# Kernel optimization log

Hardware: AMD Instinct MI355X
Metric: run time of the kernel (lower is better)

The kernel has to match this reference:

```python
import jax, jax.numpy as jnp
import numpy as np

N_NODES = 100000
N_EDGES = 1600000
IN_DIM = 128
OUT_DIM = 32
N_HEADS = 4


def setup_inputs() -> dict:
    key = jax.random.key(0)
    k1, k2, k3, k4, k5 = jax.random.split(key, 5)
    x = jax.random.normal(k1, (N_NODES, IN_DIM), dtype=jnp.float32)
    edge_index = jax.random.randint(k2, (2, N_EDGES), 0, N_NODES, dtype=jnp.int64)
    # torch nn.Linear weight layout: [out_features, in_features]
    W = jax.random.normal(k3, (OUT_DIM * N_HEADS, IN_DIM), dtype=jnp.float32) * (1.0 / np.sqrt(IN_DIM))
    a_left = jax.random.normal(k4, (N_HEADS, OUT_DIM), dtype=jnp.float32) * 0.01
    a_right = jax.random.normal(k5, (N_HEADS, OUT_DIM), dtype=jnp.float32) * 0.01
    return {"x": x, "edge_index": edge_index, "W": W, "a_left": a_left, "a_right": a_right}


def reference(x, edge_index, W, a_left, a_right):
    N = x.shape[0]
    H, D = a_left.shape
    # h: [N, H, D]
    h = (x @ W.T).reshape(N, H, D)
    src = edge_index[0]
    dst = edge_index[1]
    h_src = h[src]                                   # [E, H, D] gather
    h_dst = h[dst]                                   # [E, H, D] gather
    e = jnp.einsum('ehd,hd->eh', h_src, a_left) + jnp.einsum('ehd,hd->eh', h_dst, a_right)
    e = jax.nn.leaky_relu(e, negative_slope=0.2)
    e_exp = jnp.exp(e)                               # faithful: no max-subtraction, as in source
    denom = jax.ops.segment_sum(e_exp, dst, num_segments=N)   # [N, H]
    alpha = e_exp / (denom[dst] + 1e-8)              # [E, H]
    weighted = h_src * alpha[:, :, None]             # [E, H, D]
    out = jax.ops.segment_sum(weighted, dst, num_segments=N)  # [N, H, D]
    return out.reshape(N, H * D)                     # concat=True
```

## Files before the change

### kernel.cpp

```cpp
#include <hip/hip_runtime.h>
#include <hip/hip_bf16.h>


constexpr int IN_DIM = 128;
constexpr int HD     = 128;
constexpr int CSHIFT = 10;
constexpr int CCAP   = 17408;
constexpr int CPAD   = 16;

typedef float f32x4 __attribute__((ext_vector_type(4)));

__device__ __forceinline__ unsigned short f2bf(float f) {
  __hip_bfloat16 b = __float2bfloat16(f);
  return *(unsigned short*)&b;
}
__device__ __forceinline__ float bfl(unsigned u) { return __uint_as_float(u << 16); }
__device__ __forceinline__ float bfh(unsigned u) { return __uint_as_float(u & 0xffff0000u); }

__global__ __launch_bounds__(256)
void gemm_k(const float* __restrict__ x, const float* __restrict__ W,
            const float* __restrict__ a_left, const float* __restrict__ a_right,
            unsigned int* __restrict__ hb,
            float* __restrict__ el, float* __restrict__ er,
            int N) {
  __shared__ float xs[32][132];
  __shared__ float ws[32][132];
  const int tid = threadIdx.x;
  const int tx = tid & 15, ty = tid >> 4;
  const int n0 = blockIdx.x * 128;

  float acc[8][8];
#pragma unroll
  for (int i = 0; i < 8; ++i)
#pragma unroll
    for (int j = 0; j < 8; ++j) acc[i][j] = 0.f;

  for (int kc = 0; kc < IN_DIM; kc += 32) {
#pragma unroll
    for (int i = 0; i < 4; ++i) {
      int f  = tid + 256 * i;
      int r  = f >> 3;
      int k4 = f & 7;
      float4 xv = make_float4(0.f, 0.f, 0.f, 0.f);
      int node = n0 + r;
      if (node < N) xv = *(const float4*)&x[(size_t)node * IN_DIM + kc + 4 * k4];
      xs[4*k4+0][r] = xv.x; xs[4*k4+1][r] = xv.y; xs[4*k4+2][r] = xv.z; xs[4*k4+3][r] = xv.w;
      float4 wv = *(const float4*)&W[(size_t)r * IN_DIM + kc + 4 * k4];
      ws[4*k4+0][r] = wv.x; ws[4*k4+1][r] = wv.y; ws[4*k4+2][r] = wv.z; ws[4*k4+3][r] = wv.w;
    }
    __syncthreads();
#pragma unroll 8
    for (int kk = 0; kk < 32; ++kk) {
      float4 xa = *(const float4*)&xs[kk][8 * ty];
      float4 xb = *(const float4*)&xs[kk][8 * ty + 4];
      float4 wa = *(const float4*)&ws[kk][4 * tx];
      float4 wb = *(const float4*)&ws[kk][64 + 4 * tx];
      float xr[8] = {xa.x, xa.y, xa.z, xa.w, xb.x, xb.y, xb.z, xb.w};
      float wr[8] = {wa.x, wa.y, wa.z, wa.w, wb.x, wb.y, wb.z, wb.w};
#pragma unroll
      for (int i = 0; i < 8; ++i)
#pragma unroll
        for (int j = 0; j < 8; ++j) acc[i][j] += xr[i] * wr[j];
    }
    __syncthreads();
  }

  const int headA = tx >> 3;
  const int headB = 2 + (tx >> 3);
  const int co    = 4 * (tx & 7);
  float alA[4], arA[4], alB[4], arB[4];
#pragma unroll
  for (int j = 0; j < 4; ++j) {
    alA[j] = a_left [headA * 32 + co + j];
    arA[j] = a_right[headA * 32 + co + j];
    alB[j] = a_left [headB * 32 + co + j];
    arB[j] = a_right[headB * 32 + co + j];
  }
#pragma unroll
  for (int i = 0; i < 8; ++i) {
    int node = n0 + 8 * ty + i;
    if (node < N) {
      uint2 pA, pB;
      pA.x = ((unsigned)f2bf(acc[i][1]) << 16) | f2bf(acc[i][0]);
      pA.y = ((unsigned)f2bf(acc[i][3]) << 16) | f2bf(acc[i][2]);
      pB.x = ((unsigned)f2bf(acc[i][5]) << 16) | f2bf(acc[i][4]);
      pB.y = ((unsigned)f2bf(acc[i][7]) << 16) | f2bf(acc[i][6]);
      *(uint2*)&hb[(size_t)node * 64 + 2 * tx]      = pA;
      *(uint2*)&hb[(size_t)node * 64 + 32 + 2 * tx] = pB;
      float plA = 0.f, prA = 0.f, plB = 0.f, prB = 0.f;
#pragma unroll
      for (int j = 0; j < 4; ++j) {
        plA += acc[i][j]     * alA[j];  prA += acc[i][j]     * arA[j];
        plB += acc[i][4 + j] * alB[j];  prB += acc[i][4 + j] * arB[j];
      }
#pragma unroll
      for (int m = 1; m < 8; m <<= 1) {
        plA += __shfl_xor(plA, m, 64);  prA += __shfl_xor(prA, m, 64);
        plB += __shfl_xor(plB, m, 64);  prB += __shfl_xor(prB, m, 64);
      }
      if ((tx & 7) == 0) {
        el[node * 4 + headA] = plA;  er[node * 4 + headA] = prA;
        el[node * 4 + headB] = plB;  er[node * 4 + headB] = prB;
      }
    }
  }
}

__global__ __launch_bounds__(1024)
void binA_k(const int* __restrict__ ei, int* __restrict__ ccnt,
            unsigned* __restrict__ c1buf, int E, int ncb) {
  __shared__ unsigned staged[8192];
  __shared__ unsigned short sbin[8192];
  __shared__ int hist[128], loff[128], cur[128], gbase[128];
  __shared__ int lws[2];
  const int t = threadIdx.x;
  const int base = blockIdx.x * 8192;

  if (t < 128) hist[t] = 0;
  __syncthreads();

  int src[8], dst[8], bin[8];
#pragma unroll
  for (int i = 0; i < 8; ++i) {
    int e = base + t + 1024 * i;
    if (e < E) {
      src[i] = ei[e];
      dst[i] = ei[E + e];
      bin[i] = dst[i] >> CSHIFT;
      atomicAdd(&hist[bin[i]], 1);
    } else bin[i] = -1;
  }
  __syncthreads();

  int v = 0, s = 0;
  if (t < 128) {
    v = hist[t]; s = v;
#pragma unroll
    for (int d = 1; d < 64; d <<= 1) {
      int u = __shfl_up(s, d, 64);
      if ((t & 63) >= d) s += u;
    }
    if ((t & 63) == 63) lws[t >> 6] = s;
  }
  __syncthreads();
  if (t < 128) {
    int prefix = (t >= 64) ? lws[0] : 0;
    int excl = prefix + s - v;
    loff[t] = excl;
    cur[t]  = excl;
    gbase[t] = (t < ncb && v > 0) ? atomicAdd(&ccnt[t * CPAD], v) : 0;
  }
  __syncthreads();

#pragma unroll
  for (int i = 0; i < 8; ++i) {
    if (bin[i] >= 0) {
      int p = atomicAdd(&cur[bin[i]], 1);
      staged[p] = (unsigned)src[i] | ((unsigned)(dst[i] & 1023) << 17);
      sbin[p]   = (unsigned short)bin[i];
    }
  }
  __syncthreads();

  const int tot = loff[127] + hist[127];
  for (int j = t; j < tot; j += 1024) {
    int b = sbin[j];
    int pos = gbase[b] + (j - loff[b]);
    if (pos < CCAP) c1buf[(size_t)b * CCAP + pos] = staged[j];
  }
}

__global__ __launch_bounds__(1024)
void binB_k(const unsigned* __restrict__ c1buf, const int* __restrict__ ccnt,
            int* __restrict__ offsets, int* __restrict__ csr,
            int N, int ncb, int E) {
  __shared__ int hist[1024];
  __shared__ int wsum[16];
  __shared__ int lws2[2];
  __shared__ int sgb;
  const int b = blockIdx.x, t = threadIdx.x;
  int m = ccnt[b * CPAD];
  if (m > CCAP) m = CCAP;
  hist[t] = 0;

  int cv = 0, cs = 0;
  if (t < 128) {
    cv = (t < ncb) ? ccnt[t * CPAD] : 0;
    cs = cv;
#pragma unroll
    for (int d = 1; d < 64; d <<= 1) {
      int u = __shfl_up(cs, d, 64);
      if ((t & 63) >= d) cs += u;
    }
    if ((t & 63) == 63) lws2[t >> 6] = cs;
  }
  if (t == 0 && b == 0) offsets[N] = E;
  __syncthreads();
  if (t < 128) {
    int prefix = (t >= 64) ? lws2[0] : 0;
    if (t == b) sgb = prefix + cs - cv;
  }
  __syncthreads();
  const int gb = sgb;

  const unsigned* bp = c1buf + (size_t)b * CCAP;
  for (int i = t; i < m; i += 1024) atomicAdd(&hist[bp[i] >> 17], 1);
  __syncthreads();
  int v = hist[t], s = v;
#pragma unroll
  for (int d = 1; d < 64; d <<= 1) {
    int u = __shfl_up(s, d, 64);
    if ((t & 63) >= d) s += u;
  }
  if ((t & 63) == 63) wsum[t >> 6] = s;
  __syncthreads();
  int prefix = 0;
  for (int w = 0; w < (t >> 6); ++w) prefix += wsum[w];
  int excl = prefix + s - v;
  int node = (b << CSHIFT) + t;
  if (node < N) offsets[node] = gb + excl;
  hist[t] = excl;
  __syncthreads();
  for (int i = t; i < m; i += 1024) {
    unsigned u = bp[i];
    int r = atomicAdd(&hist[u >> 17], 1);
    csr[gb + r] = (int)(u & 0x1FFFFu);
  }
}

__global__ __launch_bounds__(256)
void agg_k(const uint4* __restrict__ hb4, const float* __restrict__ el,
           const float* __restrict__ er, const int* __restrict__ offsets,
           const int* __restrict__ csr, float* __restrict__ out, int N) {
  const int wid  = (blockIdx.x * blockDim.x + threadIdx.x) >> 6;
  const int lane = threadIdx.x & 63;
  if (wid >= N) return;
  const int start = offsets[wid];
  const int end   = offsets[wid + 1];
  const int q    = lane >> 4;
  const int ql   = lane & 15;
  const int head = ql >> 2;
  const float erv = er[wid * 4 + head];

  float a0=0.f,a1=0.f,a2=0.f,a3=0.f,a4=0.f,a5=0.f,a6=0.f,a7=0.f,den=0.f;

  for (int base = start; base < end; base += 64) {
    int lim = end - base; if (lim > 64) lim = 64;
    int ce  = base + lane;
    int creg = __builtin_nontemporal_load(&csr[(ce < end) ? ce : (end - 1)]);

    int i = 0;
    for (; i + 8 <= lim; i += 8) {
      int s0 = __shfl(creg, i + q, 64);
      int s1 = __shfl(creg, i + 4 + q, 64);
      uint4 h0 = hb4[(size_t)s0 * 16 + ql];
      uint4 h1 = hb4[(size_t)s1 * 16 + ql];
      float e0 = el[s0 * 4 + head];
      float e1 = el[s1 * 4 + head];
      float t0 = e0 + erv; t0 = (t0 > 0.f) ? t0 : 0.2f * t0;
      float t1 = e1 + erv; t1 = (t1 > 0.f) ? t1 : 0.2f * t1;
      float w0 = __expf(t0), w1 = __expf(t1);
      a0 += w0 * bfl(h0.x) + w1 * bfl(h1.x);
      a1 += w0 * bfh(h0.x) + w1 * bfh(h1.x);
      a2 += w0 * bfl(h0.y) + w1 * bfl(h1.y);
      a3 += w0 * bfh(h0.y) + w1 * bfh(h1.y);
      a4 += w0 * bfl(h0.z) + w1 * bfl(h1.z);
      a5 += w0 * bfh(h0.z) + w1 * bfh(h1.z);
      a6 += w0 * bfl(h0.w) + w1 * bfl(h1.w);
      a7 += w0 * bfh(h0.w) + w1 * bfh(h1.w);
      den += w0 + w1;
    }
    if (i < lim) {
      int i0 = i + q, i1 = i + 4 + q;
      int s0 = __shfl(creg, (i0 < lim) ? i0 : 0, 64);
      int s1 = __shfl(creg, (i1 < lim) ? i1 : 0, 64);
      uint4 h0 = hb4[(size_t)s0 * 16 + ql];
      uint4 h1 = hb4[(size_t)s1 * 16 + ql];
      float e0 = el[s0 * 4 + head];
      float e1 = el[s1 * 4 + head];
      float t0 = e0 + erv; t0 = (t0 > 0.f) ? t0 : 0.2f * t0;
      float t1 = e1 + erv; t1 = (t1 > 0.f) ? t1 : 0.2f * t1;
      float w0 = __expf(t0), w1 = __expf(t1);
      if (i0 >= lim) w0 = 0.f;
      if (i1 >= lim) w1 = 0.f;
      a0 += w0 * bfl(h0.x) + w1 * bfl(h1.x);
      a1 += w0 * bfh(h0.x) + w1 * bfh(h1.x);
      a2 += w0 * bfl(h0.y) + w1 * bfl(h1.y);
      a3 += w0 * bfh(h0.y) + w1 * bfh(h1.y);
      a4 += w0 * bfl(h0.z) + w1 * bfl(h1.z);
      a5 += w0 * bfh(h0.z) + w1 * bfh(h1.z);
      a6 += w0 * bfl(h0.w) + w1 * bfl(h1.w);
      a7 += w0 * bfh(h0.w) + w1 * bfh(h1.w);
      den += w0 + w1;
    }
  }

#pragma unroll
  for (int m = 16; m < 64; m <<= 1) {
    a0 += __shfl_xor(a0, m, 64);  a1 += __shfl_xor(a1, m, 64);
    a2 += __shfl_xor(a2, m, 64);  a3 += __shfl_xor(a3, m, 64);
    a4 += __shfl_xor(a4, m, 64);  a5 += __shfl_xor(a5, m, 64);
    a6 += __shfl_xor(a6, m, 64);  a7 += __shfl_xor(a7, m, 64);
    den += __shfl_xor(den, m, 64);
  }
  if (q == 0) {
    float inv = 1.f / (den + 1e-8f);
    f32x4 o0 = {a0 * inv, a1 * inv, a2 * inv, a3 * inv};
    f32x4 o1 = {a4 * inv, a5 * inv, a6 * inv, a7 * inv};
    __builtin_nontemporal_store(o0, (f32x4*)&out[(size_t)wid * HD + 8 * ql]);
    __builtin_nontemporal_store(o1, (f32x4*)&out[(size_t)wid * HD + 8 * ql + 4]);
  }
}

extern "C" void kernel_launch(void* const* d_in, const int* in_sizes, int n_in,
                              void* d_out, int out_size, void* d_ws, size_t ws_size,
                              hipStream_t stream) {
  const float* x       = (const float*)d_in[0];
  const int*   ei      = (const int*)d_in[1];
  const float* W       = (const float*)d_in[2];
  const float* a_left  = (const float*)d_in[3];
  const float* a_right = (const float*)d_in[4];
  float* out = (float*)d_out;

  const int N = in_sizes[0] / IN_DIM;
  const int E = in_sizes[1] / 2;
  const int NCB = (N + 1023) >> CSHIFT;

  char* p = (char*)d_ws;
  unsigned int* hb = (unsigned int*)p; p += (size_t)N * 64 * sizeof(unsigned int);
  float* el      = (float*)p; p += (size_t)N * 4 * sizeof(float);
  float* er      = (float*)p; p += (size_t)N * 4 * sizeof(float);
  int*   offsets = (int*)p;   p += (size_t)(N + 1) * sizeof(int);
  int*   ccnt    = (int*)p;   p += (size_t)NCB * CPAD * sizeof(int);
  int*   csr     = (int*)p;   p += (size_t)E * sizeof(int);
  unsigned* c1buf = (unsigned*)p; p += (size_t)NCB * CCAP * sizeof(unsigned);

  hipMemsetAsync(ccnt, 0, (size_t)NCB * CPAD * sizeof(int), stream);

  gemm_k<<<(N + 127) / 128, 256, 0, stream>>>(x, W, a_left, a_right, hb, el, er, N);
  binA_k<<<(E + 8191) / 8192, 1024, 0, stream>>>(ei, ccnt, c1buf, E, NCB);
  binB_k<<<NCB, 1024, 0, stream>>>(c1buf, ccnt, offsets, csr, N, NCB, E);
  agg_k<<<(N + 3) / 4, 256, 0, stream>>>((const uint4*)hb, el, er, offsets, csr, out, N);
}
```

Baseline: 259.3 us.

## Process four nodes per wavefront in aggregation, one quarter-wave per node

The aggregation kernel now assigns each 16-lane quarter of a wavefront its own destination node instead of splitting one node's edges across the four quarters. This removes the cross-quarter shuffle reduction and lets four nodes share a wave, so waves are no longer mostly idle on low-degree nodes. The gather address is computed with 32-bit byte offsets. The trade-off is per-wave divergence when the four nodes have different degrees, since each quarter runs its own loop length. Each quarter also now walks its edges serially, two at a time, which gives less memory-level parallelism per node.

```diff
diff --git a/kernel.cpp b/kernel.cpp
--- a/kernel.cpp
+++ b/kernel.cpp
@@ -229,37 +229,45 @@
 }
 
 __global__ __launch_bounds__(256)
-void agg_k(const uint4* __restrict__ hb4, const float* __restrict__ el,
+void agg_k(const char* __restrict__ hbc, const float* __restrict__ el,
            const float* __restrict__ er, const int* __restrict__ offsets,
            const int* __restrict__ csr, float* __restrict__ out, int N) {
-  const int wid  = (blockIdx.x * blockDim.x + threadIdx.x) >> 6;
   const int lane = threadIdx.x & 63;
-  if (wid >= N) return;
-  const int start = offsets[wid];
-  const int end   = offsets[wid + 1];
   const int q    = lane >> 4;
   const int ql   = lane & 15;
+  const int wid  = (blockIdx.x * blockDim.x + threadIdx.x) >> 6;
+  const int node = wid * 4 + q;
   const int head = ql >> 2;
-  const float erv = er[wid * 4 + head];
+  const unsigned qoff = (unsigned)(ql << 4);
+
+  int start = 0, end = 0;
+  float erv = 0.f;
+  if (node < N) {
+    start = offsets[node];
+    end   = offsets[node + 1];
+    erv   = er[node * 4 + head];
+  }
 
   float a0=0.f,a1=0.f,a2=0.f,a3=0.f,a4=0.f,a5=0.f,a6=0.f,a7=0.f,den=0.f;
 
-  for (int base = start; base < end; base += 64) {
-    int lim = end - base; if (lim > 64) lim = 64;
-    int ce  = base + lane;
-    int creg = __builtin_nontemporal_load(&csr[(ce < end) ? ce : (end - 1)]);
-
-    int i = 0;
-    for (; i + 8 <= lim; i += 8) {
-      int s0 = __shfl(creg, i + q, 64);
-      int s1 = __shfl(creg, i + 4 + q, 64);
-      uint4 h0 = hb4[(size_t)s0 * 16 + ql];
-      uint4 h1 = hb4[(size_t)s1 * 16 + ql];
+  for (int base = start; base < end; base += 16) {
+    int lim = end - base; if (lim > 16) lim = 16;
+    int ci  = base + ql;  if (ci > end - 1) ci = end - 1;
+    int creg = __builtin_nontemporal_load(&csr[ci]);
+
+    for (int i = 0; i < lim; i += 2) {
+      int i1 = (i + 1 < lim) ? (i + 1) : i;
+      int s0 = __shfl(creg, (q << 4) + i,  64);
+      int s1 = __shfl(creg, (q << 4) + i1, 64);
+      const uint4 h0 = *(const uint4*)(hbc + (((unsigned)s0 << 8) + qoff));
+      const uint4 h1 = *(const uint4*)(hbc + (((unsigned)s1 << 8) + qoff));
       float e0 = el[s0 * 4 + head];
       float e1 = el[s1 * 4 + head];
       float t0 = e0 + erv; t0 = (t0 > 0.f) ? t0 : 0.2f * t0;
       float t1 = e1 + erv; t1 = (t1 > 0.f) ? t1 : 0.2f * t1;
-      float w0 = __expf(t0), w1 = __expf(t1);
+      float w0 = __expf(t0);
+      float w1 = __expf(t1);
+      if (i + 1 >= lim) w1 = 0.f;
       a0 += w0 * bfl(h0.x) + w1 * bfl(h1.x);
       a1 += w0 * bfh(h0.x) + w1 * bfh(h1.x);
       a2 += w0 * bfl(h0.y) + w1 * bfl(h1.y);
@@ -270,45 +278,14 @@
       a7 += w0 * bfh(h0.w) + w1 * bfh(h1.w);
       den += w0 + w1;
     }
-    if (i < lim) {
-      int i0 = i + q, i1 = i + 4 + q;
-      int s0 = __shfl(creg, (i0 < lim) ? i0 : 0, 64);
-      int s1 = __shfl(creg, (i1 < lim) ? i1 : 0, 64);
-      uint4 h0 = hb4[(size_t)s0 * 16 + ql];
-      uint4 h1 = hb4[(size_t)s1 * 16 + ql];
-      float e0 = el[s0 * 4 + head];
-      float e1 = el[s1 * 4 + head];
-      float t0 = e0 + erv; t0 = (t0 > 0.f) ? t0 : 0.2f * t0;
-      float t1 = e1 + erv; t1 = (t1 > 0.f) ? t1 : 0.2f * t1;
-      float w0 = __expf(t0), w1 = __expf(t1);
-      if (i0 >= lim) w0 = 0.f;
-      if (i1 >= lim) w1 = 0.f;
-      a0 += w0 * bfl(h0.x) + w1 * bfl(h1.x);
-      a1 += w0 * bfh(h0.x) + w1 * bfh(h1.x);
-      a2 += w0 * bfl(h0.y) + w1 * bfl(h1.y);
-      a3 += w0 * bfh(h0.y) + w1 * bfh(h1.y);
-      a4 += w0 * bfl(h0.z) + w1 * bfl(h1.z);
-      a5 += w0 * bfh(h0.z) + w1 * bfh(h1.z);
-      a6 += w0 * bfl(h0.w) + w1 * bfl(h1.w);
-      a7 += w0 * bfh(h0.w) + w1 * bfh(h1.w);
-      den += w0 + w1;
-    }
-  }
-
-#pragma unroll
-  for (int m = 16; m < 64; m <<= 1) {
-    a0 += __shfl_xor(a0, m, 64);  a1 += __shfl_xor(a1, m, 64);
-    a2 += __shfl_xor(a2, m, 64);  a3 += __shfl_xor(a3, m, 64);
-    a4 += __shfl_xor(a4, m, 64);  a5 += __shfl_xor(a5, m, 64);
-    a6 += __shfl_xor(a6, m, 64);  a7 += __shfl_xor(a7, m, 64);
-    den += __shfl_xor(den, m, 64);
-  }
-  if (q == 0) {
+  }
+
+  if (node < N) {
     float inv = 1.f / (den + 1e-8f);
     f32x4 o0 = {a0 * inv, a1 * inv, a2 * inv, a3 * inv};
     f32x4 o1 = {a4 * inv, a5 * inv, a6 * inv, a7 * inv};
-    __builtin_nontemporal_store(o0, (f32x4*)&out[(size_t)wid * HD + 8 * ql]);
-    __builtin_nontemporal_store(o1, (f32x4*)&out[(size_t)wid * HD + 8 * ql + 4]);
+    __builtin_nontemporal_store(o0, (f32x4*)&out[(size_t)node * HD + 8 * ql]);
+    __builtin_nontemporal_store(o1, (f32x4*)&out[(size_t)node * HD + 8 * ql + 4]);
   }
 }
 
@@ -340,5 +317,6 @@
   gemm_k<<<(N + 127) / 128, 256, 0, stream>>>(x, W, a_left, a_right, hb, el, er, N);
   binA_k<<<(E + 8191) / 8192, 1024, 0, stream>>>(ei, ccnt, c1buf, E, NCB);
   binB_k<<<NCB, 1024, 0, stream>>>(c1buf, ccnt, offsets, csr, N, NCB, E);
-  agg_k<<<(N + 3) / 4, 256, 0, stream>>>((const uint4*)hb, el, er, offsets, csr, out, N);
-}
+
+  agg_k<<<(N + 15) / 16, 256, 0, stream>>>((const char*)hb, el, er, offsets, csr, out, N);
+}
```

Result: no change. 262.0 us (+1.0%).

## Replace two-pass binned CSR build with global histogram, scan, and atomic scatter

Applied to the files above, without the earlier changes.

The CSR construction no longer stages edges into coarse per-bin buffers. It now uses a global per-node degree histogram, a two-level prefix scan and a direct atomic scatter of source ids into the CSR array. This removes the intermediate c1buf round trip, at the cost of many global atomics on per-node counters. The scatter order within a node also becomes nondeterministic, which can change the floating-point summation order. The aggregation kernel also switches to 32-bit byte-offset address arithmetic for the gathers, aiming to cut 64-bit address computation.

```diff
diff --git a/kernel.cpp b/kernel.cpp
--- a/kernel.cpp
+++ b/kernel.cpp
@@ -5,8 +5,6 @@
 constexpr int IN_DIM = 128;
 constexpr int HD     = 128;
 constexpr int CSHIFT = 10;
-constexpr int CCAP   = 17408;
-constexpr int CPAD   = 16;
 
 typedef float f32x4 __attribute__((ext_vector_type(4)));
 
@@ -106,130 +104,76 @@
   }
 }
 
-__global__ __launch_bounds__(1024)
-void binA_k(const int* __restrict__ ei, int* __restrict__ ccnt,
-            unsigned* __restrict__ c1buf, int E, int ncb) {
-  __shared__ unsigned staged[8192];
-  __shared__ unsigned short sbin[8192];
-  __shared__ int hist[128], loff[128], cur[128], gbase[128];
+__global__ __launch_bounds__(256)
+void hist_k(const int* __restrict__ ei, int* __restrict__ cnt,
+            int* __restrict__ ccnt, int E, int ncb) {
+  __shared__ int ch[128];
+  const int t = threadIdx.x;
+  if (t < 128) ch[t] = 0;
+  __syncthreads();
+  const int stride = gridDim.x * blockDim.x;
+  for (int e = blockIdx.x * blockDim.x + t; e < E; e += stride) {
+    int d = ei[E + e];
+    atomicAdd(&cnt[d], 1);
+    atomicAdd(&ch[d >> CSHIFT], 1);
+  }
+  __syncthreads();
+  if (t < 128 && ch[t] != 0) atomicAdd(&ccnt[t], ch[t]);
+}
+
+__global__ __launch_bounds__(128)
+void cscan_k(const int* __restrict__ ccnt, int* __restrict__ cbase,
+             int* __restrict__ offsets, int ncb, int N, int E) {
   __shared__ int lws[2];
   const int t = threadIdx.x;
-  const int base = blockIdx.x * 8192;
-
-  if (t < 128) hist[t] = 0;
-  __syncthreads();
-
-  int src[8], dst[8], bin[8];
-#pragma unroll
-  for (int i = 0; i < 8; ++i) {
-    int e = base + t + 1024 * i;
-    if (e < E) {
-      src[i] = ei[e];
-      dst[i] = ei[E + e];
-      bin[i] = dst[i] >> CSHIFT;
-      atomicAdd(&hist[bin[i]], 1);
-    } else bin[i] = -1;
-  }
-  __syncthreads();
-
-  int v = 0, s = 0;
-  if (t < 128) {
-    v = hist[t]; s = v;
-#pragma unroll
-    for (int d = 1; d < 64; d <<= 1) {
-      int u = __shfl_up(s, d, 64);
-      if ((t & 63) >= d) s += u;
-    }
-    if ((t & 63) == 63) lws[t >> 6] = s;
-  }
-  __syncthreads();
-  if (t < 128) {
-    int prefix = (t >= 64) ? lws[0] : 0;
-    int excl = prefix + s - v;
-    loff[t] = excl;
-    cur[t]  = excl;
-    gbase[t] = (t < ncb && v > 0) ? atomicAdd(&ccnt[t * CPAD], v) : 0;
-  }
-  __syncthreads();
-
-#pragma unroll
-  for (int i = 0; i < 8; ++i) {
-    if (bin[i] >= 0) {
-      int p = atomicAdd(&cur[bin[i]], 1);
-      staged[p] = (unsigned)src[i] | ((unsigned)(dst[i] & 1023) << 17);
-      sbin[p]   = (unsigned short)bin[i];
-    }
-  }
-  __syncthreads();
-
-  const int tot = loff[127] + hist[127];
-  for (int j = t; j < tot; j += 1024) {
-    int b = sbin[j];
-    int pos = gbase[b] + (j - loff[b]);
-    if (pos < CCAP) c1buf[(size_t)b * CCAP + pos] = staged[j];
-  }
-}
-
-__global__ __launch_bounds__(1024)
-void binB_k(const unsigned* __restrict__ c1buf, const int* __restrict__ ccnt,
-            int* __restrict__ offsets, int* __restrict__ csr,
-            int N, int ncb, int E) {
-  __shared__ int hist[1024];
-  __shared__ int wsum[16];
-  __shared__ int lws2[2];
-  __shared__ int sgb;
-  const int b = blockIdx.x, t = threadIdx.x;
-  int m = ccnt[b * CPAD];
-  if (m > CCAP) m = CCAP;
-  hist[t] = 0;
-
-  int cv = 0, cs = 0;
-  if (t < 128) {
-    cv = (t < ncb) ? ccnt[t * CPAD] : 0;
-    cs = cv;
-#pragma unroll
-    for (int d = 1; d < 64; d <<= 1) {
-      int u = __shfl_up(cs, d, 64);
-      if ((t & 63) >= d) cs += u;
-    }
-    if ((t & 63) == 63) lws2[t >> 6] = cs;
-  }
-  if (t == 0 && b == 0) offsets[N] = E;
-  __syncthreads();
-  if (t < 128) {
-    int prefix = (t >= 64) ? lws2[0] : 0;
-    if (t == b) sgb = prefix + cs - cv;
-  }
-  __syncthreads();
-  const int gb = sgb;
-
-  const unsigned* bp = c1buf + (size_t)b * CCAP;
-  for (int i = t; i < m; i += 1024) atomicAdd(&hist[bp[i] >> 17], 1);
-  __syncthreads();
-  int v = hist[t], s = v;
+  int v = (t < ncb) ? ccnt[t] : 0;
+  int s = v;
 #pragma unroll
   for (int d = 1; d < 64; d <<= 1) {
     int u = __shfl_up(s, d, 64);
     if ((t & 63) >= d) s += u;
   }
+  if ((t & 63) == 63) lws[t >> 6] = s;
+  __syncthreads();
+  int prefix = (t >= 64) ? lws[0] : 0;
+  if (t < ncb) cbase[t] = prefix + s - v;
+  if (t == 0) offsets[N] = E;
+}
+
+__global__ __launch_bounds__(1024)
+void offs_k(const int* __restrict__ cnt, const int* __restrict__ cbase,
+            int* __restrict__ offsets, int* __restrict__ cur, int N) {
+  __shared__ int wsum[16];
+  const int b = blockIdx.x, t = threadIdx.x;
+  int v = cnt[(b << CSHIFT) + t];
+  int s = v;
+#pragma unroll
+  for (int d = 1; d < 64; d <<= 1) {
+    int u = __shfl_up(s, d, 64);
+    if ((t & 63) >= d) s += u;
+  }
   if ((t & 63) == 63) wsum[t >> 6] = s;
   __syncthreads();
   int prefix = 0;
   for (int w = 0; w < (t >> 6); ++w) prefix += wsum[w];
-  int excl = prefix + s - v;
+  int excl = cbase[b] + prefix + s - v;
   int node = (b << CSHIFT) + t;
-  if (node < N) offsets[node] = gb + excl;
-  hist[t] = excl;
-  __syncthreads();
-  for (int i = t; i < m; i += 1024) {
-    unsigned u = bp[i];
-    int r = atomicAdd(&hist[u >> 17], 1);
-    csr[gb + r] = (int)(u & 0x1FFFFu);
-  }
-}
-
-__global__ __launch_bounds__(256)
-void agg_k(const uint4* __restrict__ hb4, const float* __restrict__ el,
+  if (node < N) { offsets[node] = excl; cur[node] = excl; }
+}
+
+__global__ __launch_bounds__(256)
+void scat_k(const int* __restrict__ ei, int* __restrict__ cur,
+            int* __restrict__ csr, int E) {
+  int e = blockIdx.x * 256 + threadIdx.x;
+  if (e >= E) return;
+  int s = ei[e];
+  int d = ei[E + e];
+  int p = atomicAdd(&cur[d], 1);
+  csr[p] = s;
+}
+
+__global__ __launch_bounds__(256)
+void agg_k(const char* __restrict__ hbc, const char* __restrict__ elc,
            const float* __restrict__ er, const int* __restrict__ offsets,
            const int* __restrict__ csr, float* __restrict__ out, int N) {
   const int wid  = (blockIdx.x * blockDim.x + threadIdx.x) >> 6;
@@ -240,6 +184,8 @@
   const int q    = lane >> 4;
   const int ql   = lane & 15;
   const int head = ql >> 2;
+  const unsigned qoff = (unsigned)(ql << 4);
+  const unsigned hoff = (unsigned)(head << 2);
   const float erv = er[wid * 4 + head];
 
   float a0=0.f,a1=0.f,a2=0.f,a3=0.f,a4=0.f,a5=0.f,a6=0.f,a7=0.f,den=0.f;
@@ -253,10 +199,10 @@
     for (; i + 8 <= lim; i += 8) {
       int s0 = __shfl(creg, i + q, 64);
       int s1 = __shfl(creg, i + 4 + q, 64);
-      uint4 h0 = hb4[(size_t)s0 * 16 + ql];
-      uint4 h1 = hb4[(size_t)s1 * 16 + ql];
-      float e0 = el[s0 * 4 + head];
-      float e1 = el[s1 * 4 + head];
+      uint4 h0 = *(const uint4*)(hbc + (((unsigned)s0 << 8) + qoff));
+      uint4 h1 = *(const uint4*)(hbc + (((unsigned)s1 << 8) + qoff));
+      float e0 = *(const float*)(elc + (((unsigned)s0 << 4) + hoff));
+      float e1 = *(const float*)(elc + (((unsigned)s1 << 4) + hoff));
       float t0 = e0 + erv; t0 = (t0 > 0.f) ? t0 : 0.2f * t0;
       float t1 = e1 + erv; t1 = (t1 > 0.f) ? t1 : 0.2f * t1;
       float w0 = __expf(t0), w1 = __expf(t1);
@@ -274,10 +220,10 @@
       int i0 = i + q, i1 = i + 4 + q;
       int s0 = __shfl(creg, (i0 < lim) ? i0 : 0, 64);
       int s1 = __shfl(creg, (i1 < lim) ? i1 : 0, 64);
-      uint4 h0 = hb4[(size_t)s0 * 16 + ql];
-      uint4 h1 = hb4[(size_t)s1 * 16 + ql];
-      float e0 = el[s0 * 4 + head];
-      float e1 = el[s1 * 4 + head];
+      uint4 h0 = *(const uint4*)(hbc + (((unsigned)s0 << 8) + qoff));
+      uint4 h1 = *(const uint4*)(hbc + (((unsigned)s1 << 8) + qoff));
+      float e0 = *(const float*)(elc + (((unsigned)s0 << 4) + hoff));
+      float e1 = *(const float*)(elc + (((unsigned)s1 << 4) + hoff));
       float t0 = e0 + erv; t0 = (t0 > 0.f) ? t0 : 0.2f * t0;
       float t1 = e1 + erv; t1 = (t1 > 0.f) ? t1 : 0.2f * t1;
       float w0 = __expf(t0), w1 = __expf(t1);
@@ -325,20 +271,26 @@
   const int N = in_sizes[0] / IN_DIM;
   const int E = in_sizes[1] / 2;
   const int NCB = (N + 1023) >> CSHIFT;
+  const int NPAD = NCB << CSHIFT;
 
   char* p = (char*)d_ws;
   unsigned int* hb = (unsigned int*)p; p += (size_t)N * 64 * sizeof(unsigned int);
   float* el      = (float*)p; p += (size_t)N * 4 * sizeof(float);
   float* er      = (float*)p; p += (size_t)N * 4 * sizeof(float);
   int*   offsets = (int*)p;   p += (size_t)(N + 1) * sizeof(int);
-  int*   ccnt    = (int*)p;   p += (size_t)NCB * CPAD * sizeof(int);
+  int*   cnt     = (int*)p;   p += (size_t)NPAD * sizeof(int);
+  int*   ccnt    = (int*)p;   p += 128 * sizeof(int);
+  int*   cbase   = (int*)p;   p += 128 * sizeof(int);
+  int*   cur     = (int*)p;   p += (size_t)NPAD * sizeof(int);
   int*   csr     = (int*)p;   p += (size_t)E * sizeof(int);
-  unsigned* c1buf = (unsigned*)p; p += (size_t)NCB * CCAP * sizeof(unsigned);
-
-  hipMemsetAsync(ccnt, 0, (size_t)NCB * CPAD * sizeof(int), stream);
+
+  hipMemsetAsync(cnt, 0, ((size_t)NPAD + 128) * sizeof(int), stream);
 
   gemm_k<<<(N + 127) / 128, 256, 0, stream>>>(x, W, a_left, a_right, hb, el, er, N);
-  binA_k<<<(E + 8191) / 8192, 1024, 0, stream>>>(ei, ccnt, c1buf, E, NCB);
-  binB_k<<<NCB, 1024, 0, stream>>>(c1buf, ccnt, offsets, csr, N, NCB, E);
-  agg_k<<<(N + 3) / 4, 256, 0, stream>>>((const uint4*)hb, el, er, offsets, csr, out, N);
-}
+  hist_k<<<640, 256, 0, stream>>>(ei, cnt, ccnt, E, NCB);
+  cscan_k<<<1, 128, 0, stream>>>(ccnt, cbase, offsets, NCB, N, E);
+  offs_k<<<NCB, 1024, 0, stream>>>(cnt, cbase, offsets, cur, N);
+  scat_k<<<(E + 255) / 256, 256, 0, stream>>>(ei, cur, csr, E);
+  agg_k<<<(N + 3) / 4, 256, 0, stream>>>((const char*)hb, (const char*)el, er,
+                                         offsets, csr, out, N);
+}
```

After: 423.7 us. 63.4% more time.

## Move projection GEMM to bf16 MFMA with split hi/lo precision

Applied to the files above, without the earlier changes.

Replaces the FP32 SIMT GEMM in gemm_k with MFMA 16x16x32 bf16 instructions, using a three-term hi/lo bf16 split to approximate FP32 accuracy. Inputs are staged in swizzled LDS and W is held in registers, with 64 nodes per block. The aggregation kernel also switches to 32-bit byte-offset address arithmetic for its gathers to cut 64-bit index math. This trades some precision and extra MFMA work for matrix-core throughput; the GEMM is only part of the total, and gather/aggregation likely dominates.

```diff
diff --git a/kernel.cpp b/kernel.cpp
--- a/kernel.cpp
+++ b/kernel.cpp
@@ -9,6 +9,7 @@
 constexpr int CPAD   = 16;
 
 typedef float f32x4 __attribute__((ext_vector_type(4)));
+typedef short short8 __attribute__((ext_vector_type(8)));
 
 __device__ __forceinline__ unsigned short f2bf(float f) {
   __hip_bfloat16 b = __float2bfloat16(f);
@@ -23,84 +24,126 @@
             unsigned int* __restrict__ hb,
             float* __restrict__ el, float* __restrict__ er,
             int N) {
-  __shared__ float xs[32][132];
-  __shared__ float ws[32][132];
-  const int tid = threadIdx.x;
-  const int tx = tid & 15, ty = tid >> 4;
-  const int n0 = blockIdx.x * 128;
-
-  float acc[8][8];
-#pragma unroll
-  for (int i = 0; i < 8; ++i)
-#pragma unroll
-    for (int j = 0; j < 8; ++j) acc[i][j] = 0.f;
-
-  for (int kc = 0; kc < IN_DIM; kc += 32) {
-#pragma unroll
-    for (int i = 0; i < 4; ++i) {
-      int f  = tid + 256 * i;
-      int r  = f >> 3;
-      int k4 = f & 7;
-      float4 xv = make_float4(0.f, 0.f, 0.f, 0.f);
-      int node = n0 + r;
-      if (node < N) xv = *(const float4*)&x[(size_t)node * IN_DIM + kc + 4 * k4];
-      xs[4*k4+0][r] = xv.x; xs[4*k4+1][r] = xv.y; xs[4*k4+2][r] = xv.z; xs[4*k4+3][r] = xv.w;
-      float4 wv = *(const float4*)&W[(size_t)r * IN_DIM + kc + 4 * k4];
-      ws[4*k4+0][r] = wv.x; ws[4*k4+1][r] = wv.y; ws[4*k4+2][r] = wv.z; ws[4*k4+3][r] = wv.w;
-    }
-    __syncthreads();
-#pragma unroll 8
-    for (int kk = 0; kk < 32; ++kk) {
-      float4 xa = *(const float4*)&xs[kk][8 * ty];
-      float4 xb = *(const float4*)&xs[kk][8 * ty + 4];
-      float4 wa = *(const float4*)&ws[kk][4 * tx];
-      float4 wb = *(const float4*)&ws[kk][64 + 4 * tx];
-      float xr[8] = {xa.x, xa.y, xa.z, xa.w, xb.x, xb.y, xb.z, xb.w};
-      float wr[8] = {wa.x, wa.y, wa.z, wa.w, wb.x, wb.y, wb.z, wb.w};
-#pragma unroll
-      for (int i = 0; i < 8; ++i)
-#pragma unroll
-        for (int j = 0; j < 8; ++j) acc[i][j] += xr[i] * wr[j];
-    }
-    __syncthreads();
-  }
-
-  const int headA = tx >> 3;
-  const int headB = 2 + (tx >> 3);
-  const int co    = 4 * (tx & 7);
-  float alA[4], arA[4], alB[4], arB[4];
-#pragma unroll
-  for (int j = 0; j < 4; ++j) {
-    alA[j] = a_left [headA * 32 + co + j];
-    arA[j] = a_right[headA * 32 + co + j];
-    alB[j] = a_left [headB * 32 + co + j];
-    arB[j] = a_right[headB * 32 + co + j];
-  }
+  __shared__ __align__(16) char xs[32768];
+  const int tid  = threadIdx.x;
+  const int lane = tid & 63;
+  const int wv   = tid >> 6;
+  const int lcol = lane & 15;
+  const int lk   = lane >> 4;
+  const int n0   = blockIdx.x * 64;
+
+  short8 Bh[2][4], Bl[2][4];
+#pragma unroll
+  for (int ct = 0; ct < 2; ++ct) {
+    int col = wv * 32 + ct * 16 + lcol;
+#pragma unroll
+    for (int ks = 0; ks < 4; ++ks) {
+      int kb = ks * 32 + lk * 8;
+      const float* wp = &W[col * IN_DIM + kb];
+      float4 wa = *(const float4*)wp;
+      float4 wb = *(const float4*)(wp + 4);
+      float wf[8] = {wa.x, wa.y, wa.z, wa.w, wb.x, wb.y, wb.z, wb.w};
+      short8 uh, ul;
+#pragma unroll
+      for (int j = 0; j < 8; ++j) {
+        unsigned short hs = f2bf(wf[j]);
+        float hf = __uint_as_float((unsigned)hs << 16);
+        uh[j] = (short)hs;
+        ul[j] = (short)f2bf(wf[j] - hf);
+      }
+      Bh[ct][ks] = uh;  Bl[ct][ks] = ul;
+    }
+  }
+
 #pragma unroll
   for (int i = 0; i < 8; ++i) {
-    int node = n0 + 8 * ty + i;
-    if (node < N) {
-      uint2 pA, pB;
-      pA.x = ((unsigned)f2bf(acc[i][1]) << 16) | f2bf(acc[i][0]);
-      pA.y = ((unsigned)f2bf(acc[i][3]) << 16) | f2bf(acc[i][2]);
-      pB.x = ((unsigned)f2bf(acc[i][5]) << 16) | f2bf(acc[i][4]);
-      pB.y = ((unsigned)f2bf(acc[i][7]) << 16) | f2bf(acc[i][6]);
-      *(uint2*)&hb[(size_t)node * 64 + 2 * tx]      = pA;
-      *(uint2*)&hb[(size_t)node * 64 + 32 + 2 * tx] = pB;
-      float plA = 0.f, prA = 0.f, plB = 0.f, prB = 0.f;
-#pragma unroll
-      for (int j = 0; j < 4; ++j) {
-        plA += acc[i][j]     * alA[j];  prA += acc[i][j]     * arA[j];
-        plB += acc[i][4 + j] * alB[j];  prB += acc[i][4 + j] * arB[j];
-      }
-#pragma unroll
-      for (int m = 1; m < 8; m <<= 1) {
-        plA += __shfl_xor(plA, m, 64);  prA += __shfl_xor(prA, m, 64);
-        plB += __shfl_xor(plB, m, 64);  prB += __shfl_xor(prB, m, 64);
-      }
-      if ((tx & 7) == 0) {
-        el[node * 4 + headA] = plA;  er[node * 4 + headA] = prA;
-        el[node * 4 + headB] = plB;  er[node * 4 + headB] = prB;
+    int f  = tid + 256 * i;
+    int r  = f >> 5;
+    int c4 = f & 31;
+    int node = n0 + r;
+    float4 v = make_float4(0.f, 0.f, 0.f, 0.f);
+    if (node < N) v = *(const float4*)&x[(size_t)node * IN_DIM + c4 * 4];
+    float vf[4] = {v.x, v.y, v.z, v.w};
+    unsigned short hs[4], ls[4];
+#pragma unroll
+    for (int j = 0; j < 4; ++j) {
+      hs[j] = f2bf(vf[j]);
+      float hf = __uint_as_float((unsigned)hs[j] << 16);
+      ls[j] = f2bf(vf[j] - hf);
+    }
+    int sw = (c4 * 8) ^ ((r & 7) << 4);
+    uint2 ph = make_uint2((unsigned)hs[0] | ((unsigned)hs[1] << 16),
+                          (unsigned)hs[2] | ((unsigned)hs[3] << 16));
+    uint2 pl = make_uint2((unsigned)ls[0] | ((unsigned)ls[1] << 16),
+                          (unsigned)ls[2] | ((unsigned)ls[3] << 16));
+    *(uint2*)&xs[r * 256 + sw]         = ph;
+    *(uint2*)&xs[16384 + r * 256 + sw] = pl;
+  }
+  __syncthreads();
+
+  f32x4 acc[4][2];
+#pragma unroll
+  for (int rt = 0; rt < 4; ++rt)
+#pragma unroll
+    for (int ct = 0; ct < 2; ++ct) acc[rt][ct] = (f32x4){0.f, 0.f, 0.f, 0.f};
+
+#pragma unroll
+  for (int ks = 0; ks < 4; ++ks) {
+#pragma unroll
+    for (int rt = 0; rt < 4; ++rt) {
+      int row = rt * 16 + lcol;
+      int kb  = ks * 64 + lk * 16;
+      int ad  = row * 256 + (kb ^ ((row & 7) << 4));
+      short8 ah = *(const short8*)&xs[ad];
+      short8 al = *(const short8*)&xs[16384 + ad];
+#pragma unroll
+      for (int ct = 0; ct < 2; ++ct) {
+        acc[rt][ct] = __builtin_amdgcn_mfma_f32_16x16x32_bf16(ah, Bh[ct][ks], acc[rt][ct], 0, 0, 0);
+        acc[rt][ct] = __builtin_amdgcn_mfma_f32_16x16x32_bf16(ah, Bl[ct][ks], acc[rt][ct], 0, 0, 0);
+        acc[rt][ct] = __builtin_amdgcn_mfma_f32_16x16x32_bf16(al, Bh[ct][ks], acc[rt][ct], 0, 0, 0);
+      }
+    }
+  }
+
+  float aL[2], aR[2];
+  aL[0] = a_left [wv * 32 + lcol];  aL[1] = a_left [wv * 32 + 16 + lcol];
+  aR[0] = a_right[wv * 32 + lcol];  aR[1] = a_right[wv * 32 + 16 + lcol];
+
+#pragma unroll
+  for (int rt = 0; rt < 4; ++rt) {
+    float pl[4] = {0.f, 0.f, 0.f, 0.f}, pr[4] = {0.f, 0.f, 0.f, 0.f};
+#pragma unroll
+    for (int ct = 0; ct < 2; ++ct) {
+      float av[4] = {acc[rt][ct][0], acc[rt][ct][1], acc[rt][ct][2], acc[rt][ct][3]};
+      float pt[4];
+#pragma unroll
+      for (int r = 0; r < 4; ++r) pt[r] = __shfl_xor(av[r], 1, 64);
+      int col = wv * 32 + ct * 16 + lcol;
+      int nb  = n0 + rt * 16 + lk * 4;
+      if (!(lane & 1)) {
+#pragma unroll
+        for (int r = 0; r < 4; ++r) {
+          int node = nb + r;
+          if (node < N)
+            hb[(size_t)node * 64 + (col >> 1)] =
+                (unsigned)f2bf(av[r]) | ((unsigned)f2bf(pt[r]) << 16);
+        }
+      }
+#pragma unroll
+      for (int r = 0; r < 4; ++r) { pl[r] += av[r] * aL[ct]; pr[r] += av[r] * aR[ct]; }
+    }
+#pragma unroll
+    for (int m = 1; m < 16; m <<= 1)
+#pragma unroll
+      for (int r = 0; r < 4; ++r) {
+        pl[r] += __shfl_xor(pl[r], m, 64);
+        pr[r] += __shfl_xor(pr[r], m, 64);
+      }
+    if (lcol == 0) {
+#pragma unroll
+      for (int r = 0; r < 4; ++r) {
+        int node = n0 + rt * 16 + lk * 4 + r;
+        if (node < N) { el[node * 4 + wv] = pl[r]; er[node * 4 + wv] = pr[r]; }
       }
     }
   }
@@ -229,7 +272,7 @@
 }
 
 __global__ __launch_bounds__(256)
-void agg_k(const uint4* __restrict__ hb4, const float* __restrict__ el,
+void agg_k(const char* __restrict__ hbc, const char* __restrict__ elc,
            const float* __restrict__ er, const int* __restrict__ offsets,
            const int* __restrict__ csr, float* __restrict__ out, int N) {
   const int wid  = (blockIdx.x * blockDim.x + threadIdx.x) >> 6;
@@ -240,6 +283,8 @@
   const int q    = lane >> 4;
   const int ql   = lane & 15;
   const int head = ql >> 2;
+  const unsigned qoff = (unsigned)(ql << 4);
+  const unsigned hoff = (unsigned)(head << 2);
   const float erv = er[wid * 4 + head];
 
   float a0=0.f,a1=0.f,a2=0.f,a3=0.f,a4=0.f,a5=0.f,a6=0.f,a7=0.f,den=0.f;
@@ -253,10 +298,10 @@
     for (; i + 8 <= lim; i += 8) {
       int s0 = __shfl(creg, i + q, 64);
       int s1 = __shfl(creg, i + 4 + q, 64);
-      uint4 h0 = hb4[(size_t)s0 * 16 + ql];
-      uint4 h1 = hb4[(size_t)s1 * 16 + ql];
-      float e0 = el[s0 * 4 + head];
-      float e1 = el[s1 * 4 + head];
+      uint4 h0 = *(const uint4*)(hbc + (((unsigned)s0 << 8) + qoff));
+      uint4 h1 = *(const uint4*)(hbc + (((unsigned)s1 << 8) + qoff));
+      float e0 = *(const float*)(elc + (((unsigned)s0 << 4) + hoff));
+      float e1 = *(const float*)(elc + (((unsigned)s1 << 4) + hoff));
       float t0 = e0 + erv; t0 = (t0 > 0.f) ? t0 : 0.2f * t0;
       float t1 = e1 + erv; t1 = (t1 > 0.f) ? t1 : 0.2f * t1;
       float w0 = __expf(t0), w1 = __expf(t1);
@@ -274,10 +319,10 @@
       int i0 = i + q, i1 = i + 4 + q;
       int s0 = __shfl(creg, (i0 < lim) ? i0 : 0, 64);
       int s1 = __shfl(creg, (i1 < lim) ? i1 : 0, 64);
-      uint4 h0 = hb4[(size_t)s0 * 16 + ql];
-      uint4 h1 = hb4[(size_t)s1 * 16 + ql];
-      float e0 = el[s0 * 4 + head];
-      float e1 = el[s1 * 4 + head];
+      uint4 h0 = *(const uint4*)(hbc + (((unsigned)s0 << 8) + qoff));
+      uint4 h1 = *(const uint4*)(hbc + (((unsigned)s1 << 8) + qoff));
+      float e0 = *(const float*)(elc + (((unsigned)s0 << 4) + hoff));
+      float e1 = *(const float*)(elc + (((unsigned)s1 << 4) + hoff));
       float t0 = e0 + erv; t0 = (t0 > 0.f) ? t0 : 0.2f * t0;
       float t1 = e1 + erv; t1 = (t1 > 0.f) ? t1 : 0.2f * t1;
       float w0 = __expf(t0), w1 = __expf(t1);
@@ -337,8 +382,9 @@
 
   hipMemsetAsync(ccnt, 0, (size_t)NCB * CPAD * sizeof(int), stream);
 
-  gemm_k<<<(N + 127) / 128, 256, 0, stream>>>(x, W, a_left, a_right, hb, el, er, N);
+  gemm_k<<<(N + 63) / 64, 256, 0, stream>>>(x, W, a_left, a_right, hb, el, er, N);
   binA_k<<<(E + 8191) / 8192, 1024, 0, stream>>>(ei, ccnt, c1buf, E, NCB);
   binB_k<<<NCB, 1024, 0, stream>>>(c1buf, ccnt, offsets, csr, N, NCB, E);
-  agg_k<<<(N + 3) / 4, 256, 0, stream>>>((const uint4*)hb, el, er, offsets, csr, out, N);
-}
+  agg_k<<<(N + 3) / 4, 256, 0, stream>>>((const char*)hb, (const char*)el, er,
+                                         offsets, csr, out, N);
+}
```

Measured after the change: 238.2 us. 1.09x faster.
